# Kernel tuning notes

Hardware: AMD Instinct MI355X
Metric: run time of the kernel (lower is better)

Reference implementation:

```python
import jax, jax.numpy as jnp
import numpy as np

B, S, D, H, MEM, P = 32, 512, 768, 8, 768, 3
DK = D // H
LN_EPS = 1e-6


def _layer_norm(x, a, b):
    # torch LayerNorm in source uses unbiased std (ddof=1) and adds eps to std
    mean = x.mean(-1, keepdims=True)
    var = ((x - mean) ** 2).sum(-1, keepdims=True) / (x.shape[-1] - 1)
    return a * (x - mean) / (jnp.sqrt(var) + LN_EPS) + b


def _gcn_branch(x, mask, Wq, bq, Wk, bk, Ws, bs):
    # x: [B,S,D], mask: [B,S] 0/1 ints
    q = (x @ Wq.T + bq).reshape(B, S, H, DK).transpose(0, 2, 1, 3)  # [B,H,S,DK]
    k = (x @ Wk.T + bk).reshape(B, S, H, DK).transpose(0, 2, 1, 3)
    scores = jnp.einsum('bhqd,bhkd->bhqk', q, k) / jnp.sqrt(jnp.float32(DK))
    scores = jnp.where(mask[:, None, None, :] == 0, jnp.float32(-1e9), scores)
    adj = jax.nn.softmax(scores, axis=-1).mean(1)  # average heads -> [B,S,S]
    # adj - diag(diag(adj)) + I  ==  set diagonal to 1
    idx = jnp.arange(S)
    adj = adj.at[:, idx, idx].set(1.0)
    adj = adj * mask[:, :, None].astype(adj.dtype)  # src_mask.transpose(1,2) * adj
    denom = adj.sum(-1, keepdims=True) + 1.0
    out = x
    for W, b in zip(Ws, bs):
        out = jax.nn.relu((adj @ out @ W.T + b) / denom)
    return out, adj


def _proj(a, b):
    # Proj(a, b): (a.b / |b|) * normalize(b)
    b_mo = jnp.sqrt((b * b).sum(-1))
    axb = (a * b).sum(-1)
    bn = b / jnp.maximum(jnp.sqrt((b * b).sum(-1, keepdims=True)), 1e-12)
    return (axb / b_mo)[:, None] * bn


def setup_inputs() -> dict:
    key = jax.random.key(0)
    ks = jax.random.split(key, 32)

    def w(k, shape):
        return jax.random.normal(k, shape, jnp.float32) * 0.02

    inp = {
        'sequence_output': jax.random.normal(ks[0], (B, S, D), jnp.float32),
        'pooled_output': jax.random.normal(ks[1], (B, D), jnp.float32),
        'src_mask': jnp.ones((B, S), jnp.int32),
        'aspect_mask': jnp.ones((B, S), jnp.float32),
        'ln_a': jnp.ones((D,), jnp.float32),
        'ln_b': jnp.zeros((D,), jnp.float32),
        'fp_Wq': w(ks[2], (D, D)), 'fp_bq': jnp.zeros((D,), jnp.float32),
        'fp_Wk': w(ks[3], (D, D)), 'fp_bk': jnp.zeros((D,), jnp.float32),
        'fp_W0': w(ks[4], (MEM, D)), 'fp_b0': jnp.zeros((MEM,), jnp.float32),
        'fp_W1': w(ks[5], (MEM, MEM)), 'fp_b1': jnp.zeros((MEM,), jnp.float32),
        'fc_Wq': w(ks[6], (D, D)), 'fc_bq': jnp.zeros((D,), jnp.float32),
        'fc_Wk': w(ks[7], (D, D)), 'fc_bk': jnp.zeros((D,), jnp.float32),
        'fc_W0': w(ks[8], (MEM, D)), 'fc_b0': jnp.zeros((MEM,), jnp.float32),
        'fc_W1': w(ks[9], (MEM, MEM)), 'fc_b1': jnp.zeros((MEM,), jnp.float32),
        'fp_dense_W': w(ks[10], (P, MEM)), 'fp_dense_b': jnp.zeros((P,), jnp.float32),
        'fc_dense_W': w(ks[11], (P, MEM)), 'fc_dense_b': jnp.zeros((P,), jnp.float32),
    }
    return inp


def reference(sequence_output, pooled_output, src_mask, aspect_mask,
              ln_a, ln_b,
              fp_Wq, fp_bq, fp_Wk, fp_bk, fp_W0, fp_b0, fp_W1, fp_b1,
              fc_Wq, fc_bq, fc_Wk, fc_bk, fc_W0, fc_b0, fc_W1, fc_b1,
              fp_dense_W, fp_dense_b, fc_dense_W, fc_dense_b):
    label_embedding = pooled_output
    att_inputs = _layer_norm(sequence_output, ln_a, ln_b)  # dropout disabled (eval)
    asp_wn = aspect_mask.sum(1)[:, None]  # [B,1]

    fp_out, _ = _gcn_branch(att_inputs, src_mask, fp_Wq, fp_bq, fp_Wk, fp_bk,
                            [fp_W0, fp_W1], [fp_b0, fp_b1])
    fc_out, _ = _gcn_branch(att_inputs, src_mask, fc_Wq, fc_bq, fc_Wk, fc_bk,
                            [fc_W0, fc_W1], [fc_b0, fc_b1])

    outputs_fp = fp_out.sum(1)  # [B,MEM]
    outputs_fc = (fc_out * aspect_mask[:, :, None]).sum(1) / asp_wn  # [B,MEM]

    fp_x = _proj(outputs_fp, outputs_fc)
    fp_y = _proj(outputs_fp, outputs_fp - fp_x)
    fc_y = outputs_fc  # gradient-reverse layer is identity in forward

    logits_p = fp_y @ fp_dense_W.T + fp_dense_b
    logits_c = fc_y @ fc_dense_W.T + fc_dense_b
    return (logits_p, logits_c, fp_y, label_embedding)
```

## Files before the change

### kernel.cpp

```cpp
#include <hip/hip_runtime.h>
#include <math.h>
#include <stdint.h>

#define Bn 32
#define Sn 512
#define Dn 768
#define Hn 8
#define DKn 96
#define Pn 3

typedef __bf16 bf16_t;
typedef bf16_t bf16x8 __attribute__((ext_vector_type(8)));
typedef float f32x4 __attribute__((ext_vector_type(4)));

__device__ __forceinline__ bf16_t f2bf(float f) { return (bf16_t)f; }

__device__ __forceinline__ void gload16(const void* g, void* l) {
    __builtin_amdgcn_global_load_lds((const __attribute__((address_space(1))) void*)g,
                                     (__attribute__((address_space(3))) void*)l, 16, 0, 0);
}

__device__ __forceinline__ float brsum(float v, float* red) {
    int t = threadIdx.x;
    red[t] = v; __syncthreads();
    #pragma unroll
    for (int o = 128; o > 0; o >>= 1) {
        if (t < o) red[t] += red[t + o];
        __syncthreads();
    }
    float r = red[0]; __syncthreads();
    return r;
}

__global__ __launch_bounds__(256) void ln_kernel(const float* __restrict__ in,
                                                 const float* __restrict__ ga,
                                                 const float* __restrict__ gb,
                                                 bf16_t* __restrict__ out) {
    __shared__ float red[256];
    long row = blockIdx.x;
    const float* x = in + row * Dn;
    bf16_t* y = out + row * Dn;
    int t = threadIdx.x;
    float v0 = x[t], v1 = x[t + 256], v2 = x[t + 512];
    float mean = brsum(v0 + v1 + v2, red) / (float)Dn;
    float d0 = v0 - mean, d1 = v1 - mean, d2 = v2 - mean;
    float ss = brsum(d0 * d0 + d1 * d1 + d2 * d2, red);
    float inv = 1.0f / (sqrtf(ss / (float)(Dn - 1)) + 1e-6f);
    y[t]       = f2bf(ga[t]       * d0 * inv + gb[t]);
    y[t + 256] = f2bf(ga[t + 256] * d1 * inv + gb[t + 256]);
    y[t + 512] = f2bf(ga[t + 512] * d2 * inv + gb[t + 512]);
}

__global__ __launch_bounds__(256) void cvt8(const float* __restrict__ s0,
                                            const float* __restrict__ s1,
                                            const float* __restrict__ s2,
                                            const float* __restrict__ s3,
                                            const float* __restrict__ s4,
                                            const float* __restrict__ s5,
                                            const float* __restrict__ s6,
                                            const float* __restrict__ s7,
                                            bf16_t* __restrict__ dst) {
    int y = blockIdx.y;
    const float* s = (y == 0) ? s0 : (y == 1) ? s1 : (y == 2) ? s2 : (y == 3) ? s3
                   : (y == 4) ? s4 : (y == 5) ? s5 : (y == 6) ? s6 : s7;
    long i = (long)blockIdx.x * 1024 + threadIdx.x * 4;
    float4 v = *reinterpret_cast<const float4*>(s + i);
    bf16_t* d = dst + (long)y * Dn * Dn + i;
    d[0] = f2bf(v.x); d[1] = f2bf(v.y); d[2] = f2bf(v.z); d[3] = f2bf(v.w);
}

__global__ __launch_bounds__(256) void biascat_k(const float* __restrict__ s0,
                                                 const float* __restrict__ s1,
                                                 const float* __restrict__ s2,
                                                 const float* __restrict__ s3,
                                                 const float* __restrict__ s4,
                                                 const float* __restrict__ s5,
                                                 const float* __restrict__ s6,
                                                 const float* __restrict__ s7,
                                                 float* __restrict__ dst) {
    int y = blockIdx.x;
    const float* s = (y == 0) ? s0 : (y == 1) ? s1 : (y == 2) ? s2 : (y == 3) ? s3
                   : (y == 4) ? s4 : (y == 5) ? s5 : (y == 6) ? s6 : s7;
    for (int i = threadIdx.x; i < Dn; i += 256) dst[(long)y * Dn + i] = s[i];
}

__global__ void zero_kernel(float* p, int n) {
    int i = blockIdx.x * 256 + threadIdx.x;
    if (i < n) p[i] = 0.0f;
}

template <int EPI>
__global__ __launch_bounds__(256) void gemm_bt(
    const bf16_t* __restrict__ Ag, const bf16_t* __restrict__ Bg,
    bf16_t* __restrict__ Cg, float* __restrict__ outv,
    int lda, int ldb, int ldc, int K,
    long sAhi, long sAlo, long sBhi, long sBlo, long sChi, long sClo,
    int lgZ, float alpha,
    const float* __restrict__ bias, long bias_zs,
    const float* __restrict__ denom,
    const float* __restrict__ aspw) {
    __shared__ __align__(16) bf16_t As[128 * 32];
    __shared__ __align__(16) bf16_t Bs[128 * 32];

    unsigned gx = gridDim.x, gy = gridDim.y;
    unsigned nwg = gx * gy * gridDim.z;
    unsigned flat = (blockIdx.z * gy + blockIdx.y) * gx + blockIdx.x;
    unsigned q8 = nwg >> 3, r8 = nwg & 7;
    unsigned xcd = flat & 7, idx = flat >> 3;
    unsigned swz = (xcd < r8 ? xcd * (q8 + 1) : r8 * (q8 + 1) + (xcd - r8) * q8) + idx;
    unsigned bx = swz % gx;
    unsigned rest = swz / gx;
    unsigned by = rest % gy;
    unsigned zz = rest / gy;
    int zb = zz >> lgZ;
    int zg = zz & ((1 << lgZ) - 1);
    long zful = zz;

    const bf16_t* A = Ag + zb * sAhi + zg * sAlo;
    const bf16_t* B = Bg + zb * sBhi + zg * sBlo;

    int n0 = bx * 128;
    int m0 = by * 128;
    int tid = threadIdx.x;
    int lane = tid & 63, wv = tid >> 6;
    int wm = wv >> 1, wn = wv & 1;

    int sub = lane >> 2;
    int kcol = (lane & 3) * 8;
    const bf16_t* pA0 = A + (size_t)(m0 + wv * 16 + sub) * lda + kcol;
    const bf16_t* pA1 = pA0 + (size_t)64 * lda;
    const bf16_t* pB0 = B + (size_t)(n0 + wv * 16 + sub) * ldb + kcol;
    const bf16_t* pB1 = pB0 + (size_t)64 * ldb;
    bf16_t* lA0 = As + wv * 512 + lane * 8;
    bf16_t* lA1 = As + (4 + wv) * 512 + lane * 8;
    bf16_t* lB0 = Bs + wv * 512 + lane * 8;
    bf16_t* lB1 = Bs + (4 + wv) * 512 + lane * 8;

    f32x4 acc[4][4];
    #pragma unroll
    for (int i = 0; i < 4; i++)
        #pragma unroll
        for (int j = 0; j < 4; j++) acc[i][j] = (f32x4){0.f, 0.f, 0.f, 0.f};

    const bf16_t* ar = As + (wm * 64 + (lane & 15)) * 32 + (lane >> 4) * 8;
    const bf16_t* br = Bs + (wn * 64 + (lane & 15)) * 32 + (lane >> 4) * 8;

    for (int k0 = 0; k0 < K; k0 += 32) {
        gload16(pA0 + k0, lA0);
        gload16(pA1 + k0, lA1);
        gload16(pB0 + k0, lB0);
        gload16(pB1 + k0, lB1);
        __syncthreads();
        bf16x8 a[4], b[4];
        #pragma unroll
        for (int i = 0; i < 4; i++) a[i] = *(const bf16x8*)(ar + i * 16 * 32);
        #pragma unroll
        for (int j = 0; j < 4; j++) b[j] = *(const bf16x8*)(br + j * 16 * 32);
        #pragma unroll
        for (int i = 0; i < 4; i++)
            #pragma unroll
            for (int j = 0; j < 4; j++)
                acc[i][j] = __builtin_amdgcn_mfma_f32_16x16x32_bf16(a[i], b[j], acc[i][j], 0, 0, 0);
        __syncthreads();
    }

    int nb = n0 + wn * 64 + (lane & 15);
    int mbase = m0 + wm * 64 + (lane >> 4) * 4;
    const float* bz = bias ? bias + zb * bias_zs : nullptr;

    if (EPI == 0) {
        bf16_t* Cz = Cg + zb * sChi + zg * sClo;
        #pragma unroll
        for (int i = 0; i < 4; i++) {
            #pragma unroll
            for (int r = 0; r < 4; r++) {
                long m = mbase + i * 16 + r;
                bf16_t* crow = Cz + m * (long)ldc;
                #pragma unroll
                for (int j = 0; j < 4; j++) {
                    int col = nb + j * 16;
                    float v = acc[i][j][r] * alpha;
                    if (bz) v += bz[col];
                    crow[col] = f2bf(v);
                }
            }
        }
    } else if (EPI == 1) {
        bf16_t* Cz = Cg + zb * sChi + zg * sClo;
        const float* dz = denom + zful * Sn;
        #pragma unroll
        for (int i = 0; i < 4; i++) {
            #pragma unroll
            for (int r = 0; r < 4; r++) {
                int m = mbase + i * 16 + r;
                float dinv = 1.0f / dz[m];
                bf16_t* crow = Cz + (long)m * ldc;
                #pragma unroll
                for (int j = 0; j < 4; j++) {
                    float v = fmaxf((acc[i][j][r] + bz[nb + j * 16]) * dinv, 0.0f);
                    crow[nb + j * 16] = f2bf(v);
                }
            }
        }
    } else {
        const float* dz = denom + zful * Sn;
        float csum[4] = {0.f, 0.f, 0.f, 0.f};
        #pragma unroll
        for (int i = 0; i < 4; i++) {
            #pragma unroll
            for (int r = 0; r < 4; r++) {
                int m = mbase + i * 16 + r;
                float dinv = 1.0f / dz[m];
                float wgt = (aspw && zb) ? aspw[(long)zg * Sn + m] : 1.0f;
                #pragma unroll
                for (int j = 0; j < 4; j++) {
                    float v = fmaxf((acc[i][j][r] + bz[nb + j * 16]) * dinv, 0.0f);
                    csum[j] += v * wgt;
                }
            }
        }
        #pragma unroll
        for (int j = 0; j < 4; j++) {
            float s = csum[j];
            s += __shfl_xor(s, 16);
            s += __shfl_xor(s, 32);
            if (lane < 16) atomicAdd(&outv[zful * Dn + nb + j * 16], s);
        }
    }
}

template <int EPI>
__global__ __launch_bounds__(512, 1) void gemm256(
    const bf16_t* __restrict__ Ag, const bf16_t* __restrict__ Bg,
    bf16_t* __restrict__ Cg, float* __restrict__ outv,
    int lda, int ldb, int ldc, int K,
    long sAhi, long sAlo, long sBhi, long sBlo, long sChi, long sClo,
    int lgZ,
    const float* __restrict__ bias, long bias_zs,
    const float* __restrict__ denom,
    const float* __restrict__ aspw) {
    __shared__ __align__(16) bf16_t lds[4][2][8192];

    unsigned gx = gridDim.x, gy = gridDim.y;
    unsigned nwg = gx * gy * gridDim.z;
    unsigned flat = (blockIdx.z * gy + blockIdx.y) * gx + blockIdx.x;
    unsigned q8 = nwg >> 3, r8 = nwg & 7;
    unsigned xcd = flat & 7, idx = flat >> 3;
    unsigned swz = (xcd < r8 ? xcd * (q8 + 1) : r8 * (q8 + 1) + (xcd - r8) * q8) + idx;
    unsigned bx = swz % gx;
    unsigned rest = swz / gx;
    unsigned by = rest % gy;
    unsigned zz = rest / gy;
    int zb = zz >> lgZ;
    int zg = zz & ((1 << lgZ) - 1);

    const bf16_t* A = Ag + zb * sAhi + zg * sAlo;
    const bf16_t* B = Bg + zb * sBhi + zg * sBlo;

    int n0 = bx * 256, m0 = by * 256;
    int tid = threadIdx.x;
    int lane = tid & 63, w = tid >> 6;
    int wm = w >> 2, wn = w & 3;

    const int NT = K >> 5;

    int srow = lane & 15;
    int skc = (lane >> 4) * 8;
    const bf16_t* Asrc0 = A + (size_t)(m0 + (w * 2 + 0) * 16 + srow) * lda + skc;
    const bf16_t* Asrc1 = A + (size_t)(m0 + (w * 2 + 1) * 16 + srow) * lda + skc;
    const bf16_t* Bsrc0 = B + (size_t)(n0 + (w * 2 + 0) * 16 + srow) * ldb + skc;
    const bf16_t* Bsrc1 = B + (size_t)(n0 + (w * 2 + 1) * 16 + srow) * ldb + skc;
    int c0off = (w * 2 + 0) * 512 + lane * 8;
    int c1off = (w * 2 + 1) * 512 + lane * 8;

    f32x4 acc[8][4];
    #pragma unroll
    for (int i = 0; i < 8; ++i)
        #pragma unroll
        for (int j = 0; j < 4; ++j) acc[i][j] = (f32x4){0.f, 0.f, 0.f, 0.f};

    #pragma unroll
    for (int tt = 0; tt < 3; ++tt) {
        gload16(Asrc0 + tt * 32, &lds[tt][0][c0off]);
        gload16(Asrc1 + tt * 32, &lds[tt][0][c1off]);
        gload16(Bsrc0 + tt * 32, &lds[tt][1][c0off]);
        gload16(Bsrc1 + tt * 32, &lds[tt][1][c1off]);
    }
    asm volatile("s_waitcnt vmcnt(8)" ::: "memory");
    __builtin_amdgcn_s_barrier();

    int aoff = wm * 8 * 512 + lane * 8;
    int boff = wn * 4 * 512 + lane * 8;

    for (int t = 0; t < NT; ++t) {
        const bf16_t* bufA = &lds[t & 3][0][0];
        const bf16_t* bufB = &lds[t & 3][1][0];
        int tn = t + 3;
        bf16_t* dA = &lds[tn & 3][0][0];
        bf16_t* dB = &lds[tn & 3][1][0];
        bool st = tn < NT;

        bf16x8 a[4], b[4];
        #pragma unroll
        for (int i = 0; i < 4; ++i)
            a[i] = *(const bf16x8*)(bufA + aoff + i * 512);
        #pragma unroll
        for (int j = 0; j < 4; ++j)
            b[j] = *(const bf16x8*)(bufB + boff + j * 512);
        if (st) {
            gload16(Asrc0 + tn * 32, dA + c0off);
            gload16(Bsrc0 + tn * 32, dB + c0off);
        }
        __builtin_amdgcn_s_barrier();
        asm volatile("s_waitcnt lgkmcnt(0)" ::: "memory");
        __builtin_amdgcn_sched_barrier(0);
        __builtin_amdgcn_s_setprio(1);
        #pragma unroll
        for (int i = 0; i < 4; ++i)
            #pragma unroll
            for (int j = 0; j < 4; ++j)
                acc[i][j] = __builtin_amdgcn_mfma_f32_16x16x32_bf16(a[i], b[j], acc[i][j], 0, 0, 0);
        __builtin_amdgcn_s_setprio(0);
        __builtin_amdgcn_s_barrier();

        #pragma unroll
        for (int i = 0; i < 4; ++i)
            a[i] = *(const bf16x8*)(bufA + aoff + (4 + i) * 512);
        if (st) {
            gload16(Asrc1 + tn * 32, dA + c1off);
            gload16(Bsrc1 + tn * 32, dB + c1off);
        }
        __builtin_amdgcn_s_barrier();
        asm volatile("s_waitcnt lgkmcnt(0)" ::: "memory");
        __builtin_amdgcn_sched_barrier(0);
        __builtin_amdgcn_s_setprio(1);
        #pragma unroll
        for (int i = 0; i < 4; ++i)
            #pragma unroll
            for (int j = 0; j < 4; ++j)
                acc[4 + i][j] = __builtin_amdgcn_mfma_f32_16x16x32_bf16(a[i], b[j], acc[4 + i][j], 0, 0, 0);
        __builtin_amdgcn_s_setprio(0);
        if (t + 3 < NT)      asm volatile("s_waitcnt vmcnt(8)" ::: "memory");
        else if (t + 2 < NT) asm volatile("s_waitcnt vmcnt(4)" ::: "memory");
        else                 asm volatile("s_waitcnt vmcnt(0)" ::: "memory");
        __builtin_amdgcn_s_barrier();
    }

    int nb = n0 + wn * 64 + (lane & 15);
    int mbase = m0 + wm * 128 + (lane >> 4) * 4;
    const float* bz = bias ? bias + zb * bias_zs : nullptr;

    if (EPI == 0) {
        bf16_t* Cz = Cg + zb * sChi + zg * sClo;
        #pragma unroll
        for (int i = 0; i < 8; ++i) {
            #pragma unroll
            for (int r = 0; r < 4; ++r) {
                long m = mbase + i * 16 + r;
                bf16_t* crow = Cz + m * (long)ldc;
                #pragma unroll
                for (int j = 0; j < 4; ++j) {
                    int col = nb + j * 16;
                    float v = acc[i][j][r];
                    if (bz) v += bz[col];
                    crow[col] = f2bf(v);
                }
            }
        }
    }
}

#define KPAD 100
__global__ __launch_bounds__(256) void fused_adj(
    const bf16_t* __restrict__ QK, bf16_t* __restrict__ adjb,
    float* __restrict__ denomv, const int* __restrict__ mask) {
    __shared__ __align__(16) bf16_t Ks[2][128 * KPAD];
    __shared__ float red[4][16];

    int L = blockIdx.x;
    int swzi = (L & 7) * 128 + (L >> 3);
    int brc = swzi >> 9;
    int rem = swzi & 511;
    int b = rem >> 4;
    int q0 = (rem & 15) * 32;

    int tid = threadIdx.x;
    int lane = tid & 63, w = tid >> 6;
    int mt = w >> 1, nh = w & 1;
    int g = lane >> 4, c = lane & 15;

    const int LDQ = 3072;
    const bf16_t* Qrow  = QK + ((long)b * Sn + q0 + mt * 16 + c) * LDQ + brc * 1536;
    const bf16_t* Kbase = QK + (long)b * Sn * LDQ + brc * 1536 + Dn;

    const int* mrow = mask + (long)b * Sn;
    unsigned mbits = 0;
    #pragma unroll
    for (int t = 0; t < 4; ++t)
        #pragma unroll
        for (int nj = 0; nj < 4; ++nj)
            if (mrow[t * 128 + nh * 64 + nj * 16 + c] != 0) mbits |= 1u << (t * 4 + nj);

    int srow[6], scc[6];
    #pragma unroll
    for (int p = 0; p < 6; ++p) { int gr = tid + p * 256; srow[p] = gr / 12; scc[p] = gr % 12; }

    f32x4 adjacc[4][4];
    #pragma unroll
    for (int t = 0; t < 4; ++t)
        #pragma unroll
        for (int nj = 0; nj < 4; ++nj) adjacc[t][nj] = (f32x4){0.f, 0.f, 0.f, 0.f};

    f32x4 S[4][4];
    bf16x8 kr0[6], kr1[6], aq[3], aqn[3];
    const float sal = 0.102062072615966f;

    #pragma unroll
    for (int p = 0; p < 6; ++p)
        kr0[p] = *(const bf16x8*)(Kbase + (long)srow[p] * LDQ + scc[p] * 8);
    #pragma unroll
    for (int ks = 0; ks < 3; ++ks)
        aq[ks] = *(const bf16x8*)(Qrow + ks * 32 + g * 8);
    #pragma unroll
    for (int p = 0; p < 6; ++p)
        *(bf16x8*)(&Ks[0][srow[p] * KPAD + scc[p] * 8]) = kr0[p];
    #pragma unroll
    for (int p = 0; p < 6; ++p)
        kr1[p] = *(const bf16x8*)(Kbase + (long)(128 + srow[p]) * LDQ + scc[p] * 8);
    __syncthreads();

    for (int h = 0; h < Hn; ++h) {
        #pragma unroll
        for (int t = 0; t < 4; ++t)
            #pragma unroll
            for (int nj = 0; nj < 4; ++nj) S[t][nj] = (f32x4){0.f, 0.f, 0.f, 0.f};

        float rs[4];
        #pragma unroll
        for (int t = 0; t < 4; ++t) {
            int it = h * 4 + t;
            if (it + 2 < 32) {
                int nt = it + 2;
                const bf16_t* kp = Kbase + (long)((nt & 3) * 128) * LDQ + (nt >> 2) * 96;
                if ((t & 1) == 0) {
                    #pragma unroll
                    for (int p = 0; p < 6; ++p)
                        kr0[p] = *(const bf16x8*)(kp + (long)srow[p] * LDQ + scc[p] * 8);
                } else {
                    #pragma unroll
                    for (int p = 0; p < 6; ++p)
                        kr1[p] = *(const bf16x8*)(kp + (long)srow[p] * LDQ + scc[p] * 8);
                }
            }
            if (t == 2 && h < 7) {
                #pragma unroll
                for (int ks = 0; ks < 3; ++ks)
                    aqn[ks] = *(const bf16x8*)(Qrow + (h + 1) * 96 + ks * 32 + g * 8);
            }
            #pragma unroll
            for (int nj = 0; nj < 4; ++nj) {
                #pragma unroll
                for (int ks = 0; ks < 3; ++ks) {
                    bf16x8 bk = *(const bf16x8*)(&Ks[t & 1][(nh * 64 + nj * 16 + c) * KPAD + ks * 32 + g * 8]);
                    S[t][nj] = __builtin_amdgcn_mfma_f32_16x16x32_bf16(aq[ks], bk, S[t][nj], 0, 0, 0);
                }
            }
            if (t == 3) {
                rs[0] = rs[1] = rs[2] = rs[3] = 0.f;
                #pragma unroll
                for (int tt = 0; tt < 4; ++tt)
                    #pragma unroll
                    for (int nj = 0; nj < 4; ++nj) {
                        float mkf = ((mbits >> (tt * 4 + nj)) & 1u) ? 1.0f : 0.0f;
                        #pragma unroll
                        for (int ri = 0; ri < 4; ++ri) {
                            float e = mkf * __expf(S[tt][nj][ri] * sal);
                            S[tt][nj][ri] = e;
                            rs[ri] += e;
                        }
                    }
                #pragma unroll
                for (int ri = 0; ri < 4; ++ri) {
                    rs[ri] += __shfl_xor(rs[ri], 1);
                    rs[ri] += __shfl_xor(rs[ri], 2);
                    rs[ri] += __shfl_xor(rs[ri], 4);
                    rs[ri] += __shfl_xor(rs[ri], 8);
                }
                if (c == 0) {
                    #pragma unroll
                    for (int ri = 0; ri < 4; ++ri) red[w][g * 4 + ri] = rs[ri];
                }
            }
            if (it + 1 < 32) {
                if ((t & 1) == 0) {
                    #pragma unroll
                    for (int p = 0; p < 6; ++p)
                        *(bf16x8*)(&Ks[1][srow[p] * KPAD + scc[p] * 8]) = kr1[p];
                } else {
                    #pragma unroll
                    for (int p = 0; p < 6; ++p)
                        *(bf16x8*)(&Ks[0][srow[p] * KPAD + scc[p] * 8]) = kr0[p];
                }
            }
            __syncthreads();
            if (t == 3) {
                float inv[4];
                #pragma unroll
                for (int ri = 0; ri < 4; ++ri)
                    inv[ri] = 0.125f / (red[w][g * 4 + ri] + red[w ^ 1][g * 4 + ri]);
                #pragma unroll
                for (int tt = 0; tt < 4; ++tt)
                    #pragma unroll
                    for (int nj = 0; nj < 4; ++nj)
                        #pragma unroll
                        for (int ri = 0; ri < 4; ++ri)
                            adjacc[tt][nj][ri] += S[tt][nj][ri] * inv[ri];
                if (h < 7) {
                    #pragma unroll
                    for (int ks = 0; ks < 3; ++ks) aq[ks] = aqn[ks];
                }
            }
        }
    }

    float rm[4];
    #pragma unroll
    for (int ri = 0; ri < 4; ++ri)
        rm[ri] = (mrow[q0 + mt * 16 + g * 4 + ri] != 0) ? 1.0f : 0.0f;
    float rs2[4] = {0.f, 0.f, 0.f, 0.f};
    #pragma unroll
    for (int t = 0; t < 4; ++t)
        #pragma unroll
        for (int nj = 0; nj < 4; ++nj) {
            int n = t * 128 + nh * 64 + nj * 16 + c;
            #pragma unroll
            for (int ri = 0; ri < 4; ++ri) {
                float v = adjacc[t][nj][ri];
                int q = q0 + mt * 16 + g * 4 + ri;
                if (n == q) v = 1.0f;
                v *= rm[ri];
                adjacc[t][nj][ri] = v;
                rs2[ri] += v;
            }
        }
    #pragma unroll
    for (int ri = 0; ri < 4; ++ri) {
        rs2[ri] += __shfl_xor(rs2[ri], 1);
        rs2[ri] += __shfl_xor(rs2[ri], 2);
        rs2[ri] += __shfl_xor(rs2[ri], 4);
        rs2[ri] += __shfl_xor(rs2[ri], 8);
    }
    __syncthreads();
    if (c == 0) {
        #pragma unroll
        for (int ri = 0; ri < 4; ++ri) red[w][g * 4 + ri] = rs2[ri];
    }
    __syncthreads();
    long zful = (long)brc * Bn + b;
    if (nh == 0 && c == 0) {
        #pragma unroll
        for (int ri = 0; ri < 4; ++ri)
            denomv[zful * Sn + q0 + mt * 16 + g * 4 + ri] =
                red[w][g * 4 + ri] + red[w ^ 1][g * 4 + ri] + 1.0f;
    }
    bf16_t* stg = &Ks[0][0];
    #pragma unroll
    for (int t = 0; t < 4; ++t)
        #pragma unroll
        for (int nj = 0; nj < 4; ++nj) {
            int n = t * 128 + nh * 64 + nj * 16 + c;
            #pragma unroll
            for (int ri = 0; ri < 4; ++ri)
                stg[(mt * 16 + g * 4 + ri) * 520 + n] = f2bf(adjacc[t][nj][ri]);
        }
    __syncthreads();
    bf16_t* arow = adjb + (zful * Sn + q0) * Sn;
    #pragma unroll
    for (int p = 0; p < 8; ++p) {
        int gr = tid + p * 256;
        int row = gr >> 6, cc = gr & 63;
        *(bf16x8*)(arow + (long)row * Sn + cc * 8) = *(const bf16x8*)(stg + row * 520 + cc * 8);
    }
}

__global__ __launch_bounds__(256) void final_kernel(const float* __restrict__ ofp,
                                                    const float* __restrict__ ofc_raw,
                                                    const float* __restrict__ aspect,
                                                    const float* __restrict__ pooled,
                                                    const float* __restrict__ fpdW,
                                                    const float* __restrict__ fpdb,
                                                    const float* __restrict__ fcdW,
                                                    const float* __restrict__ fcdb,
                                                    float* __restrict__ out) {
    __shared__ float red[256];
    __shared__ float fp[Dn], fc[Dn], fy[Dn];
    int b = blockIdx.x, t = threadIdx.x;
    float awv = aspect[(long)b * Sn + t] + aspect[(long)b * Sn + t + 256];
    float asp_wn = brsum(awv, red);
    for (int i = t; i < Dn; i += 256) {
        fp[i] = ofp[(long)b * Dn + i];
        fc[i] = ofc_raw[(long)b * Dn + i] / asp_wn;
    }
    __syncthreads();
    float p0 = 0.0f, p1 = 0.0f;
    for (int i = t; i < Dn; i += 256) { p0 += fc[i] * fc[i]; p1 += fp[i] * fc[i]; }
    float dfc2 = brsum(p0, red);
    float dfpfc = brsum(p1, red);
    float bmo = sqrtf(dfc2);
    float coef = dfpfc / bmo;
    float bden = fmaxf(bmo, 1e-12f);
    float q0 = 0.0f, q1 = 0.0f;
    for (int i = t; i < Dn; i += 256) {
        float tv = fp[i] - coef * fc[i] / bden;
        fy[i] = tv;
        q0 += tv * tv;
        q1 += fp[i] * tv;
    }
    float dt2 = brsum(q0, red);
    float dfpt = brsum(q1, red);
    float tmo = sqrtf(dt2);
    float coef2 = dfpt / tmo;
    float tden = fmaxf(tmo, 1e-12f);
    for (int i = t; i < Dn; i += 256) fy[i] = coef2 * fy[i] / tden;
    __syncthreads();
    for (int i = t; i < Dn; i += 256) out[2 * Bn * Pn + (long)b * Dn + i] = fy[i];
    for (int i = t; i < Dn; i += 256)
        out[2 * Bn * Pn + Bn * Dn + (long)b * Dn + i] = pooled[(long)b * Dn + i];
    for (int j = 0; j < Pn; j++) {
        float lp = 0.0f, lc = 0.0f;
        for (int i = t; i < Dn; i += 256) {
            lp += fy[i] * fpdW[(long)j * Dn + i];
            lc += fc[i] * fcdW[(long)j * Dn + i];
        }
        float rp = brsum(lp, red);
        float rc = brsum(lc, red);
        if (t == 0) {
            out[(long)b * Pn + j] = rp + fpdb[j];
            out[Bn * Pn + (long)b * Pn + j] = rc + fcdb[j];
        }
    }
}

extern "C" void kernel_launch(void* const* d_in, const int* in_sizes, int n_in,
                              void* d_out, int out_size, void* d_ws, size_t ws_size,
                              hipStream_t stream) {
    const float* seq     = (const float*)d_in[0];
    const float* pooled  = (const float*)d_in[1];
    const int*   src_msk = (const int*)d_in[2];
    const float* aspect  = (const float*)d_in[3];
    const float* ln_a    = (const float*)d_in[4];
    const float* ln_b    = (const float*)d_in[5];
    float* out = (float*)d_out;

    const long NTD = (long)Bn * Sn * Dn;
    const long NSS = (long)Bn * Sn * Sn;
    const long DD  = (long)Dn * Dn;
    const long SD  = (long)Sn * Dn;

    char* w = (char*)d_ws;
    bf16_t* xbf   = (bf16_t*)w;
    bf16_t* QK    = xbf + NTD;
    bf16_t* H1    = QK;
    bf16_t* XT    = QK + 2 * NTD;
    bf16_t* adjb  = QK + 4 * NTD;
    float*  denom = (float*)(adjb + 2 * NSS);
    float*  ofp   = denom + 2L * Bn * Sn;
    float*  bcat  = ofp + 2L * Bn * Dn;
    bf16_t* Wb    = (bf16_t*)(bcat + 8 * Dn);

    ln_kernel<<<dim3(Bn * Sn), dim3(256), 0, stream>>>(seq, ln_a, ln_b, xbf);
    zero_kernel<<<dim3((2 * Bn * Dn + 255) / 256), dim3(256), 0, stream>>>(ofp, 2 * Bn * Dn);

    cvt8<<<dim3(576, 8), dim3(256), 0, stream>>>(
        (const float*)d_in[6], (const float*)d_in[8],
        (const float*)d_in[14], (const float*)d_in[16],
        (const float*)d_in[10], (const float*)d_in[18],
        (const float*)d_in[12], (const float*)d_in[20], Wb);
    biascat_k<<<dim3(8), dim3(256), 0, stream>>>(
        (const float*)d_in[7], (const float*)d_in[9],
        (const float*)d_in[15], (const float*)d_in[17],
        (const float*)d_in[11], (const float*)d_in[19],
        (const float*)d_in[13], (const float*)d_in[21], bcat);

    gemm256<0><<<dim3(12, 64, 1), dim3(512), 0, stream>>>(
        xbf, Wb, QK, nullptr, Dn, Dn, 3072, Dn,
        0, 0, 0, 0, 0, 0, 0, bcat, 0, nullptr, nullptr);

    fused_adj<<<dim3(2 * Bn * Sn / 32), dim3(256), 0, stream>>>(QK, adjb, denom, src_msk);

    gemm_bt<0><<<dim3(4, 6, 64), dim3(256), 0, stream>>>(
        Wb + 4 * DD, xbf, XT, nullptr, Dn, Dn, Sn, Dn,
        DD, 0, 0, SD, 32 * SD, SD,
        5, 1.0f, nullptr, 0, nullptr, nullptr);

    gemm_bt<1><<<dim3(6, 4, 64), dim3(256), 0, stream>>>(
        adjb, XT, H1, nullptr, Sn, Sn, Dn, Sn,
        32L * Sn * Sn, (long)Sn * Sn, 32 * SD, SD, 32 * SD, SD,
        5, 1.0f, bcat + 4 * Dn, Dn, denom, nullptr);

    gemm_bt<0><<<dim3(4, 6, 64), dim3(256), 0, stream>>>(
        Wb + 6 * DD, H1, XT, nullptr, Dn, Dn, Sn, Dn,
        DD, 0, 32 * SD, SD, 32 * SD, SD,
        5, 1.0f, nullptr, 0, nullptr, nullptr);

    gemm_bt<2><<<dim3(6, 4, 64), dim3(256), 0, stream>>>(
        adjb, XT, nullptr, ofp, Sn, Sn, 0, Sn,
        32L * Sn * Sn, (long)Sn * Sn, 32 * SD, SD, 0, 0,
        5, 1.0f, bcat + 6 * Dn, Dn, denom, aspect);

    final_kernel<<<dim3(Bn), dim3(256), 0, stream>>>(
        ofp, ofp + (long)Bn * Dn, aspect, pooled,
        (const float*)d_in[22], (const float*)d_in[23],
        (const float*)d_in[24], (const float*)d_in[25], out);
}
```

Before: 507.0 us.

## Shrink QK projection GEMM tile to 256x128 with 3-stage LDS ring

The QK projection GEMM tile narrows from 256x256 to 256x128, and the grid doubles along N. The LDS ring drops from four stages to three, which cuts shared memory to about 72KB and allows higher occupancy (launch bounds now permit 4 blocks). Each wave now does a single 4x4 MFMA block per k-step instead of two halves, with a simpler prefetch and barrier schedule. Relu/denominator epilogue variants are also added, but only EPI 0 is launched. The trade-off is less operand reuse per tile in exchange for more blocks and more latency hiding.

```diff
diff --git a/kernel.cpp b/kernel.cpp
--- a/kernel.cpp
+++ b/kernel.cpp
@@ -229,8 +229,9 @@
     }
 }
 
+#define CH 24
 template <int EPI>
-__global__ __launch_bounds__(512, 1) void gemm256(
+__global__ __launch_bounds__(512, 4) void gemm256(
     const bf16_t* __restrict__ Ag, const bf16_t* __restrict__ Bg,
     bf16_t* __restrict__ Cg, float* __restrict__ outv,
     int lda, int ldb, int ldc, int K,
@@ -239,7 +240,7 @@
     const float* __restrict__ bias, long bias_zs,
     const float* __restrict__ denom,
     const float* __restrict__ aspw) {
-    __shared__ __align__(16) bf16_t lds[4][2][8192];
+    __shared__ __align__(16) bf16_t lds[3][CH * 512];
 
     unsigned gx = gridDim.x, gy = gridDim.y;
     unsigned nwg = gx * gy * gridDim.z;
@@ -253,65 +254,62 @@
     unsigned zz = rest / gy;
     int zb = zz >> lgZ;
     int zg = zz & ((1 << lgZ) - 1);
+    long zful = zz;
 
     const bf16_t* A = Ag + zb * sAhi + zg * sAlo;
     const bf16_t* B = Bg + zb * sBhi + zg * sBlo;
 
-    int n0 = bx * 256, m0 = by * 256;
+    int n0 = bx * 128, m0 = by * 256;
     int tid = threadIdx.x;
     int lane = tid & 63, w = tid >> 6;
-    int wm = w >> 2, wn = w & 3;
+    int wm = w >> 1, wn = w & 1;
 
     const int NT = K >> 5;
 
-    int srow = lane & 15;
+    int srowl = lane & 15;
     int skc = (lane >> 4) * 8;
-    const bf16_t* Asrc0 = A + (size_t)(m0 + (w * 2 + 0) * 16 + srow) * lda + skc;
-    const bf16_t* Asrc1 = A + (size_t)(m0 + (w * 2 + 1) * 16 + srow) * lda + skc;
-    const bf16_t* Bsrc0 = B + (size_t)(n0 + (w * 2 + 0) * 16 + srow) * ldb + skc;
-    const bf16_t* Bsrc1 = B + (size_t)(n0 + (w * 2 + 1) * 16 + srow) * ldb + skc;
-    int c0off = (w * 2 + 0) * 512 + lane * 8;
-    int c1off = (w * 2 + 1) * 512 + lane * 8;
-
-    f32x4 acc[8][4];
-    #pragma unroll
-    for (int i = 0; i < 8; ++i)
+    const bf16_t* src[3];
+    int loff[3];
+    #pragma unroll
+    for (int p = 0; p < 3; ++p) {
+        int ch = w * 3 + p;
+        src[p] = (ch < 16) ? (A + (size_t)(m0 + ch * 16 + srowl) * lda + skc)
+                           : (B + (size_t)(n0 + (ch - 16) * 16 + srowl) * ldb + skc);
+        loff[p] = ch * 512 + lane * 8;
+    }
+
+    f32x4 acc[4][4];
+    #pragma unroll
+    for (int i = 0; i < 4; ++i)
         #pragma unroll
         for (int j = 0; j < 4; ++j) acc[i][j] = (f32x4){0.f, 0.f, 0.f, 0.f};
 
     #pragma unroll
-    for (int tt = 0; tt < 3; ++tt) {
-        gload16(Asrc0 + tt * 32, &lds[tt][0][c0off]);
-        gload16(Asrc1 + tt * 32, &lds[tt][0][c1off]);
-        gload16(Bsrc0 + tt * 32, &lds[tt][1][c0off]);
-        gload16(Bsrc1 + tt * 32, &lds[tt][1][c1off]);
-    }
-    asm volatile("s_waitcnt vmcnt(8)" ::: "memory");
+    for (int p = 0; p < 3; ++p) gload16(src[p], &lds[0][loff[p]]);
+    if (NT > 1) {
+        #pragma unroll
+        for (int p = 0; p < 3; ++p) gload16(src[p] + 32, &lds[1][loff[p]]);
+        asm volatile("s_waitcnt vmcnt(3)" ::: "memory");
+    } else {
+        asm volatile("s_waitcnt vmcnt(0)" ::: "memory");
+    }
     __builtin_amdgcn_s_barrier();
 
-    int aoff = wm * 8 * 512 + lane * 8;
-    int boff = wn * 4 * 512 + lane * 8;
+    int aoff = (wm * 4) * 512 + lane * 8;
+    int boff = (16 + wn * 4) * 512 + lane * 8;
 
     for (int t = 0; t < NT; ++t) {
-        const bf16_t* bufA = &lds[t & 3][0][0];
-        const bf16_t* bufB = &lds[t & 3][1][0];
-        int tn = t + 3;
-        bf16_t* dA = &lds[tn & 3][0][0];
-        bf16_t* dB = &lds[tn & 3][1][0];
-        bool st = tn < NT;
-
+        const bf16_t* buf = &lds[t % 3][0];
+        if (t + 2 < NT) {
+            bf16_t* dst = &lds[(t + 2) % 3][0];
+            #pragma unroll
+            for (int p = 0; p < 3; ++p) gload16(src[p] + (t + 2) * 32, dst + loff[p]);
+        }
         bf16x8 a[4], b[4];
         #pragma unroll
-        for (int i = 0; i < 4; ++i)
-            a[i] = *(const bf16x8*)(bufA + aoff + i * 512);
-        #pragma unroll
-        for (int j = 0; j < 4; ++j)
-            b[j] = *(const bf16x8*)(bufB + boff + j * 512);
-        if (st) {
-            gload16(Asrc0 + tn * 32, dA + c0off);
-            gload16(Bsrc0 + tn * 32, dB + c0off);
-        }
-        __builtin_amdgcn_s_barrier();
+        for (int i = 0; i < 4; ++i) a[i] = *(const bf16x8*)(buf + aoff + i * 512);
+        #pragma unroll
+        for (int j = 0; j < 4; ++j) b[j] = *(const bf16x8*)(buf + boff + j * 512);
         asm volatile("s_waitcnt lgkmcnt(0)" ::: "memory");
         __builtin_amdgcn_sched_barrier(0);
         __builtin_amdgcn_s_setprio(1);
@@ -321,39 +319,19 @@
             for (int j = 0; j < 4; ++j)
                 acc[i][j] = __builtin_amdgcn_mfma_f32_16x16x32_bf16(a[i], b[j], acc[i][j], 0, 0, 0);
         __builtin_amdgcn_s_setprio(0);
+        if (t + 2 < NT) asm volatile("s_waitcnt vmcnt(3)" ::: "memory");
+        else            asm volatile("s_waitcnt vmcnt(0)" ::: "memory");
         __builtin_amdgcn_s_barrier();
-
-        #pragma unroll
-        for (int i = 0; i < 4; ++i)
-            a[i] = *(const bf16x8*)(bufA + aoff + (4 + i) * 512);
-        if (st) {
-            gload16(Asrc1 + tn * 32, dA + c1off);
-            gload16(Bsrc1 + tn * 32, dB + c1off);
-        }
-        __builtin_amdgcn_s_barrier();
-        asm volatile("s_waitcnt lgkmcnt(0)" ::: "memory");
-        __builtin_amdgcn_sched_barrier(0);
-        __builtin_amdgcn_s_setprio(1);
-        #pragma unroll
-        for (int i = 0; i < 4; ++i)
-            #pragma unroll
-            for (int j = 0; j < 4; ++j)
-                acc[4 + i][j] = __builtin_amdgcn_mfma_f32_16x16x32_bf16(a[i], b[j], acc[4 + i][j], 0, 0, 0);
-        __builtin_amdgcn_s_setprio(0);
-        if (t + 3 < NT)      asm volatile("s_waitcnt vmcnt(8)" ::: "memory");
-        else if (t + 2 < NT) asm volatile("s_waitcnt vmcnt(4)" ::: "memory");
-        else                 asm volatile("s_waitcnt vmcnt(0)" ::: "memory");
-        __builtin_amdgcn_s_barrier();
     }
 
     int nb = n0 + wn * 64 + (lane & 15);
-    int mbase = m0 + wm * 128 + (lane >> 4) * 4;
+    int mbase = m0 + wm * 64 + (lane >> 4) * 4;
     const float* bz = bias ? bias + zb * bias_zs : nullptr;
 
     if (EPI == 0) {
         bf16_t* Cz = Cg + zb * sChi + zg * sClo;
         #pragma unroll
-        for (int i = 0; i < 8; ++i) {
+        for (int i = 0; i < 4; ++i) {
             #pragma unroll
             for (int r = 0; r < 4; ++r) {
                 long m = mbase + i * 16 + r;
@@ -366,6 +344,47 @@
                     crow[col] = f2bf(v);
                 }
             }
+        }
+    } else if (EPI == 1) {
+        bf16_t* Cz = Cg + zb * sChi + zg * sClo;
+        const float* dz = denom + zful * Sn;
+        #pragma unroll
+        for (int i = 0; i < 4; ++i) {
+            #pragma unroll
+            for (int r = 0; r < 4; ++r) {
+                int m = mbase + i * 16 + r;
+                float dinv = 1.0f / dz[m];
+                bf16_t* crow = Cz + (long)m * ldc;
+                #pragma unroll
+                for (int j = 0; j < 4; ++j) {
+                    float v = fmaxf((acc[i][j][r] + bz[nb + j * 16]) * dinv, 0.0f);
+                    crow[nb + j * 16] = f2bf(v);
+                }
+            }
+        }
+    } else {
+        const float* dz = denom + zful * Sn;
+        float csum[4] = {0.f, 0.f, 0.f, 0.f};
+        #pragma unroll
+        for (int i = 0; i < 4; ++i) {
+            #pragma unroll
+            for (int r = 0; r < 4; ++r) {
+                int m = mbase + i * 16 + r;
+                float dinv = 1.0f / dz[m];
+                float wgt = (aspw && zb) ? aspw[(long)zg * Sn + m] : 1.0f;
+                #pragma unroll
+                for (int j = 0; j < 4; ++j) {
+                    float v = fmaxf((acc[i][j][r] + bz[nb + j * 16]) * dinv, 0.0f);
+                    csum[j] += v * wgt;
+                }
+            }
+        }
+        #pragma unroll
+        for (int j = 0; j < 4; ++j) {
+            float s = csum[j];
+            s += __shfl_xor(s, 16);
+            s += __shfl_xor(s, 32);
+            if (lane < 16) atomicAdd(&outv[zful * Dn + nb + j * 16], s);
         }
     }
 }
@@ -682,7 +701,7 @@
         (const float*)d_in[11], (const float*)d_in[19],
         (const float*)d_in[13], (const float*)d_in[21], bcat);
 
-    gemm256<0><<<dim3(12, 64, 1), dim3(512), 0, stream>>>(
+    gemm256<0><<<dim3(24, 64, 1), dim3(512), 0, stream>>>(
         xbf, Wb, QK, nullptr, Dn, Dn, 3072, Dn,
         0, 0, 0, 0, 0, 0, 0, bcat, 0, nullptr, nullptr);
 
```

Result: no change. 498.3 us (median of 2 runs) (-1.7%).
